# Kernel tuning notes

Measured on AMD Instinct MI355X. Metric: run time of the kernel, lower is better.

## Reference

```python
import jax, jax.numpy as jnp
import numpy as np

B, T, C = 16, 2048, 1024
HEAD = 64

def setup_inputs() -> dict:
    key = jax.random.key(0)
    kx, kq, kk, kv = jax.random.split(key, 4)
    x = jax.random.normal(kx, (B, T, C), dtype=jnp.float32)
    s = 1.0 / np.sqrt(C)
    Wq = jax.random.normal(kq, (C, HEAD), dtype=jnp.float32) * s
    Wk = jax.random.normal(kk, (C, HEAD), dtype=jnp.float32) * s
    Wv = jax.random.normal(kv, (C, HEAD), dtype=jnp.float32) * s
    return {"x": x, "Wq": Wq, "Wk": Wk, "Wv": Wv}

def reference(x, Wq, Wk, Wv):
    Bb, Tt, Cc = x.shape
    q = jnp.einsum('btc,ch->bth', x, Wq)  # [B,T,H]
    k = jnp.einsum('btc,ch->bth', x, Wk)
    v = jnp.einsum('btc,ch->bth', x, Wv)
    # NOTE: source scales by C**-0.5 (n_embd), not head_size**-0.5
    scores = jnp.einsum('bth,bsh->bts', q, k) * (Cc ** -0.5)  # [B,T,T]
    causal = jnp.tril(jnp.ones((Tt, Tt), dtype=bool))
    scores = jnp.where(causal, scores, -jnp.inf)
    attn = jax.nn.softmax(scores, axis=-1)  # dropout p=0 -> identity
    out = jnp.einsum('bts,bsh->bth', attn, v)  # [B,T,H]
    return out
```

## Files before the change

### kernel.cpp

```cpp
#include <hip/hip_runtime.h>

typedef __bf16 bf16;
typedef __bf16 bf16x4 __attribute__((ext_vector_type(4)));
typedef __bf16 bf16x8 __attribute__((ext_vector_type(8)));
typedef float f32x4 __attribute__((ext_vector_type(4)));

#define TT_ 2048
#define CC_ 1024
#define HH_ 64

#define SCALE2 0.045084221f

__global__ __launch_bounds__(256) void prep_w(const float* __restrict__ Wq,
                                              const float* __restrict__ Wk,
                                              const float* __restrict__ Wv,
                                              bf16* __restrict__ Wt) {
    __shared__ bf16 Ls[64 * 65];
    const int m  = blockIdx.x >> 4;
    const int k0 = (blockIdx.x & 15) * 64;
    const float* W = (m == 0) ? Wq : (m == 1) ? Wk : Wv;
    const int tid = threadIdx.x;
    #pragma unroll
    for (int j = 0; j < 4; ++j) {
        int idx = tid + 256 * j;
        int r   = idx >> 4;
        int c4  = (idx & 15) * 4;
        float4 w = *(const float4*)&W[(size_t)(k0 + r) * HH_ + c4];
        Ls[r * 65 + c4 + 0] = (bf16)w.x;
        Ls[r * 65 + c4 + 1] = (bf16)w.y;
        Ls[r * 65 + c4 + 2] = (bf16)w.z;
        Ls[r * 65 + c4 + 3] = (bf16)w.w;
    }
    __syncthreads();
    #pragma unroll
    for (int j = 0; j < 4; ++j) {
        int idx = tid + 256 * j;
        int n   = idx >> 4;
        int kc  = (idx & 15) * 4;
        bf16x4 v;
        #pragma unroll
        for (int i = 0; i < 4; ++i) v[i] = Ls[(kc + i) * 65 + n];
        *(bf16x4*)&Wt[m * 65536 + n * 1024 + k0 + kc] = v;
    }
}

__global__ __launch_bounds__(256) void qkv_kernel(const float* __restrict__ x,
                                                  const bf16* __restrict__ Wt,
                                                  bf16* __restrict__ qb,
                                                  bf16* __restrict__ kb,
                                                  bf16* __restrict__ vt) {
    __shared__ __align__(16) bf16 Xs[2][64 * 72];
    const int tid  = threadIdx.x;
    const int wave = tid >> 6;
    const int lane = tid & 15;
    const int quad = (tid & 63) >> 4;
    const int m0   = blockIdx.x * 64;

    f32x4 acc[4][3];
    #pragma unroll
    for (int i = 0; i < 4; ++i)
        #pragma unroll
        for (int j = 0; j < 3; ++j) acc[i][j] = f32x4{0.f, 0.f, 0.f, 0.f};

    const int srow = tid >> 4;
    const int scol = (tid & 15) * 4;

    float4 xr[4];
    #pragma unroll
    for (int rr = 0; rr < 4; ++rr)
        xr[rr] = *(const float4*)&x[(size_t)(m0 + srow + rr * 16) * CC_ + scol];
    #pragma unroll
    for (int rr = 0; rr < 4; ++rr) {
        bf16x4 bv = {(bf16)xr[rr].x, (bf16)xr[rr].y, (bf16)xr[rr].z, (bf16)xr[rr].w};
        *(bf16x4*)&Xs[0][(srow + rr * 16) * 72 + scol] = bv;
    }

    for (int kbi = 0; kbi < 16; ++kbi) {
        const int cur = kbi & 1;
        const int k0  = kbi * 64;
        __syncthreads();
        if (kbi < 15) {
            #pragma unroll
            for (int rr = 0; rr < 4; ++rr)
                xr[rr] = *(const float4*)&x[(size_t)(m0 + srow + rr * 16) * CC_ + k0 + 64 + scol];
        }
        bf16x8 bfr[2][3];
        #pragma unroll
        for (int step = 0; step < 2; ++step)
            #pragma unroll
            for (int ct = 0; ct < 3; ++ct)
                bfr[step][ct] = *(const bf16x8*)&Wt[(size_t)(wave * 48 + ct * 16 + lane) * 1024 + k0 + step * 32 + quad * 8];
        bf16x8 afr[2][4];
        #pragma unroll
        for (int step = 0; step < 2; ++step)
            #pragma unroll
            for (int rt = 0; rt < 4; ++rt)
                afr[step][rt] = *(const bf16x8*)&Xs[cur][(rt * 16 + lane) * 72 + step * 32 + quad * 8];
        #pragma unroll
        for (int step = 0; step < 2; ++step)
            #pragma unroll
            for (int ct = 0; ct < 3; ++ct)
                #pragma unroll
                for (int rt = 0; rt < 4; ++rt)
                    acc[rt][ct] = __builtin_amdgcn_mfma_f32_16x16x32_bf16(afr[step][rt], bfr[step][ct], acc[rt][ct], 0, 0, 0);
        if (kbi < 15) {
            #pragma unroll
            for (int rr = 0; rr < 4; ++rr) {
                bf16x4 bv = {(bf16)xr[rr].x, (bf16)xr[rr].y, (bf16)xr[rr].z, (bf16)xr[rr].w};
                *(bf16x4*)&Xs[cur ^ 1][(srow + rr * 16) * 72 + scol] = bv;
            }
        }
    }

    const int bb = m0 >> 11;
    const int t0 = m0 & 2047;
    __syncthreads();
    #pragma unroll
    for (int ct = 0; ct < 3; ++ct) {
        int c0 = wave * 48 + ct * 16;
        if (c0 < 128) {
            bf16* outp = (c0 < 64) ? qb : kb;
            int h = (c0 & 63) + lane;
            #pragma unroll
            for (int rt = 0; rt < 4; ++rt)
                #pragma unroll
                for (int r = 0; r < 4; ++r)
                    outp[(size_t)(m0 + rt * 16 + quad * 4 + r) * HH_ + h] = (bf16)acc[rt][ct][r];
        } else {
            int h = (c0 - 128) + lane;
            #pragma unroll
            for (int rt = 0; rt < 4; ++rt)
                #pragma unroll
                for (int r = 0; r < 4; ++r)
                    Xs[0][(rt * 16 + quad * 4 + r) * 72 + h] = (bf16)acc[rt][ct][r];
        }
    }
    __syncthreads();
    {
        int h  = tid >> 2;
        int tc = (tid & 3) * 16;
        bf16x8 v0, v1;
        #pragma unroll
        for (int i = 0; i < 8; ++i) v0[i] = Xs[0][(tc + i) * 72 + h];
        #pragma unroll
        for (int i = 0; i < 8; ++i) v1[i] = Xs[0][(tc + 8 + i) * 72 + h];
        bf16* dst = &vt[(size_t)bb * HH_ * TT_ + (size_t)h * TT_ + t0 + tc];
        *(bf16x8*)dst = v0;
        *(bf16x8*)(dst + 8) = v1;
    }
}

__global__ __launch_bounds__(256) void attn_kernel(const bf16* __restrict__ qb,
                                                   const bf16* __restrict__ kb,
                                                   const bf16* __restrict__ vt,
                                                   bf16* __restrict__ PO,
                                                   float* __restrict__ PL) {
    __shared__ __align__(16) bf16 Ks[128 * 72];
    __shared__ __align__(16) bf16 Vs[64 * 136];
    __shared__ __align__(16) bf16 Ps[4][16 * 136];

    const int tid  = threadIdx.x;
    const int wave = tid >> 6;
    const int lane = tid & 15;
    const int quad = (tid & 63) >> 4;
    const int idx = blockIdx.x;
    const int bb  = blockIdx.y;
    int seg, qi;
    if (idx < 32)      { seg = 0; qi = idx; }
    else if (idx < 56) { seg = 1; qi = idx - 24; }
    else if (idx < 72) { seg = 2; qi = idx - 40; }
    else               { seg = 3; qi = idx - 48; }
    const int q0   = qi * 64;
    const int qrow = q0 + wave * 16;
    const int nch   = (seg < (qi >> 3)) ? 4 : (((qi & 7) + 2) >> 1);
    const int diagc = (seg == (qi >> 3)) ? nch - 1 : -1;

    bf16x8 aq[2];
    #pragma unroll
    for (int step = 0; step < 2; ++step)
        aq[step] = *(const bf16x8*)&qb[(size_t)(bb * TT_ + qrow + lane) * HH_ + step * 32 + quad * 8];

    f32x4 o_acc[4];
    #pragma unroll
    for (int ht = 0; ht < 4; ++ht) o_acc[ht] = f32x4{0.f, 0.f, 0.f, 0.f};
    float l_lane[4] = {0.f, 0.f, 0.f, 0.f};

    for (int c = 0; c < nch; ++c) {
        const int s0 = seg * 512 + c * 128;
        __syncthreads();
        #pragma unroll
        for (int j = 0; j < 4; ++j) {
            int ch = tid + 256 * j;
            int row = ch >> 3, c8 = (ch & 7) * 8;
            *(bf16x8*)&Ks[row * 72 + c8] =
                *(const bf16x8*)&kb[(size_t)(bb * TT_ + s0 + row) * HH_ + c8];
        }
        #pragma unroll
        for (int j = 0; j < 4; ++j) {
            int ch = tid + 256 * j;
            int h = ch >> 4, c8 = (ch & 15) * 8;
            *(bf16x8*)&Vs[h * 136 + c8] =
                *(const bf16x8*)&vt[(size_t)bb * HH_ * TT_ + (size_t)h * TT_ + s0 + c8];
        }
        __syncthreads();

        f32x4 sfr[8];
        #pragma unroll
        for (int nt = 0; nt < 8; ++nt) sfr[nt] = f32x4{0.f, 0.f, 0.f, 0.f};
        #pragma unroll
        for (int step = 0; step < 2; ++step)
            #pragma unroll
            for (int nt = 0; nt < 8; ++nt) {
                bf16x8 bk = *(const bf16x8*)&Ks[(nt * 16 + lane) * 72 + step * 32 + quad * 8];
                sfr[nt] = __builtin_amdgcn_mfma_f32_16x16x32_bf16(aq[step], bk, sfr[nt], 0, 0, 0);
            }

        const bool msk = (c == diagc);
        #pragma unroll
        for (int r = 0; r < 4; ++r) {
            const int rowg = qrow + quad * 4 + r;
            #pragma unroll
            for (int nt = 0; nt < 8; ++nt) {
                float e = __builtin_amdgcn_exp2f(sfr[nt][r] * SCALE2);
                if (msk && (s0 + nt * 16 + lane) > rowg) e = 0.f;
                sfr[nt][r] = e;
                l_lane[r] += e;
            }
        }

        #pragma unroll
        for (int nt = 0; nt < 8; ++nt)
            #pragma unroll
            for (int r = 0; r < 4; ++r)
                Ps[wave][(quad * 4 + r) * 136 + nt * 16 + lane] = (bf16)sfr[nt][r];

        #pragma unroll
        for (int step = 0; step < 4; ++step) {
            bf16x8 ap = *(const bf16x8*)&Ps[wave][lane * 136 + step * 32 + quad * 8];
            #pragma unroll
            for (int ht = 0; ht < 4; ++ht) {
                bf16x8 bv = *(const bf16x8*)&Vs[(ht * 16 + lane) * 136 + step * 32 + quad * 8];
                o_acc[ht] = __builtin_amdgcn_mfma_f32_16x16x32_bf16(ap, bv, o_acc[ht], 0, 0, 0);
            }
        }
    }

    const size_t p = (size_t)bb * 80 + idx;
    #pragma unroll
    for (int ht = 0; ht < 4; ++ht)
        #pragma unroll
        for (int r = 0; r < 4; ++r)
            PO[p * 4096 + (size_t)(wave * 16 + quad * 4 + r) * 64 + ht * 16 + lane] = (bf16)o_acc[ht][r];
    #pragma unroll
    for (int r = 0; r < 4; ++r) {
        float l = l_lane[r];
        l += __shfl_xor(l, 1);
        l += __shfl_xor(l, 2);
        l += __shfl_xor(l, 4);
        l += __shfl_xor(l, 8);
        if (lane == 0) PL[p * 64 + wave * 16 + quad * 4 + r] = l;
    }
}

__global__ __launch_bounds__(256) void combine_kernel(const bf16* __restrict__ PO,
                                                      const float* __restrict__ PL,
                                                      float* __restrict__ out) {
    const int qi = blockIdx.x, bb = blockIdx.y;
    const int tid = threadIdx.x;
    const int r  = tid >> 2;
    const int cb = (tid & 3) * 16;
    const int ns = (qi >> 3) + 1;
    const int off[4] = {0, 32, 56, 72};

    float acc[16];
    #pragma unroll
    for (int i = 0; i < 16; ++i) acc[i] = 0.f;
    float l = 0.f;
    for (int s = 0; s < ns; ++s) {
        const size_t p = (size_t)bb * 80 + off[s] + qi - 8 * s;
        l += PL[p * 64 + r];
        const bf16* po = &PO[p * 4096 + (size_t)r * 64 + cb];
        bf16x8 a0 = *(const bf16x8*)po;
        bf16x8 a1 = *(const bf16x8*)(po + 8);
        #pragma unroll
        for (int i = 0; i < 8; ++i) { acc[i] += (float)a0[i]; acc[8 + i] += (float)a1[i]; }
    }
    const float inv = 1.0f / l;
    float* dst = &out[(size_t)(bb * TT_ + qi * 64 + r) * HH_ + cb];
    #pragma unroll
    for (int v = 0; v < 4; ++v) {
        float4 o = {acc[v * 4] * inv, acc[v * 4 + 1] * inv, acc[v * 4 + 2] * inv, acc[v * 4 + 3] * inv};
        *(float4*)(dst + v * 4) = o;
    }
}

extern "C" void kernel_launch(void* const* d_in, const int* in_sizes, int n_in,
                              void* d_out, int out_size, void* d_ws, size_t ws_size,
                              hipStream_t stream) {
    const float* x  = (const float*)d_in[0];
    const float* Wq = (const float*)d_in[1];
    const float* Wk = (const float*)d_in[2];
    const float* Wv = (const float*)d_in[3];
    float* out = (float*)d_out;

    char* ws = (char*)d_ws;
    bf16*  qb = (bf16*)(ws);
    bf16*  kb = (bf16*)(ws + 4194304);
    bf16*  vt = (bf16*)(ws + 8388608);
    bf16*  Wt = (bf16*)(ws + 12582912);
    bf16*  PO = (bf16*)(ws + 12976128);
    float* PL = (float*)(ws + 23461888);

    prep_w<<<48, 256, 0, stream>>>(Wq, Wk, Wv, Wt);
    qkv_kernel<<<512, 256, 0, stream>>>(x, Wt, qb, kb, vt);
    attn_kernel<<<dim3(80, 16), 256, 0, stream>>>(qb, kb, vt, PO, PL);
    combine_kernel<<<dim3(32, 16), 256, 0, stream>>>(PO, PL, out);
}
```

Baseline: 258.6 us.

## Load x directly into registers in QKV, halve rows per block, alias P with K in LDS

The QKV projection now uses 32 rows per block across twice as many blocks. Each wave loads and converts its x fragments straight from global memory instead of staging them through double-buffered shared memory, and a min-blocks launch bound is added. In attention, the per-wave P buffer now reuses the K tile's shared memory, with an extra barrier, to cut LDS footprint and raise occupancy. The cost is redundant global reads of x across the four waves (relying on cache) and an additional synchronisation per chunk.

```diff
diff --git a/kernel.cpp b/kernel.cpp
--- a/kernel.cpp
+++ b/kernel.cpp
@@ -44,77 +44,56 @@
     }
 }
 
-__global__ __launch_bounds__(256) void qkv_kernel(const float* __restrict__ x,
-                                                  const bf16* __restrict__ Wt,
-                                                  bf16* __restrict__ qb,
-                                                  bf16* __restrict__ kb,
-                                                  bf16* __restrict__ vt) {
-    __shared__ __align__(16) bf16 Xs[2][64 * 72];
+__global__ __launch_bounds__(256, 4) void qkv_kernel(const float* __restrict__ x,
+                                                     const bf16* __restrict__ Wt,
+                                                     bf16* __restrict__ qb,
+                                                     bf16* __restrict__ kb,
+                                                     bf16* __restrict__ vt) {
+    __shared__ __align__(16) bf16 Vsm[32 * 72];
     const int tid  = threadIdx.x;
     const int wave = tid >> 6;
     const int lane = tid & 15;
     const int quad = (tid & 63) >> 4;
-    const int m0   = blockIdx.x * 64;
-
-    f32x4 acc[4][3];
-    #pragma unroll
-    for (int i = 0; i < 4; ++i)
+    const int m0   = blockIdx.x * 32;
+
+    f32x4 acc[2][3];
+    #pragma unroll
+    for (int i = 0; i < 2; ++i)
         #pragma unroll
         for (int j = 0; j < 3; ++j) acc[i][j] = f32x4{0.f, 0.f, 0.f, 0.f};
 
-    const int srow = tid >> 4;
-    const int scol = (tid & 15) * 4;
-
-    float4 xr[4];
-    #pragma unroll
-    for (int rr = 0; rr < 4; ++rr)
-        xr[rr] = *(const float4*)&x[(size_t)(m0 + srow + rr * 16) * CC_ + scol];
-    #pragma unroll
-    for (int rr = 0; rr < 4; ++rr) {
-        bf16x4 bv = {(bf16)xr[rr].x, (bf16)xr[rr].y, (bf16)xr[rr].z, (bf16)xr[rr].w};
-        *(bf16x4*)&Xs[0][(srow + rr * 16) * 72 + scol] = bv;
-    }
-
+    #pragma unroll 4
     for (int kbi = 0; kbi < 16; ++kbi) {
-        const int cur = kbi & 1;
-        const int k0  = kbi * 64;
-        __syncthreads();
-        if (kbi < 15) {
-            #pragma unroll
-            for (int rr = 0; rr < 4; ++rr)
-                xr[rr] = *(const float4*)&x[(size_t)(m0 + srow + rr * 16) * CC_ + k0 + 64 + scol];
-        }
+        const int k0 = kbi * 64;
+        bf16x8 afr[2][2];
+        #pragma unroll
+        for (int rt = 0; rt < 2; ++rt)
+            #pragma unroll
+            for (int step = 0; step < 2; ++step) {
+                const float* xp = &x[(size_t)(m0 + rt * 16 + lane) * CC_ + k0 + step * 32 + quad * 8];
+                float4 a0 = *(const float4*)xp;
+                float4 a1 = *(const float4*)(xp + 4);
+                bf16x8 af = {(bf16)a0.x, (bf16)a0.y, (bf16)a0.z, (bf16)a0.w,
+                             (bf16)a1.x, (bf16)a1.y, (bf16)a1.z, (bf16)a1.w};
+                afr[rt][step] = af;
+            }
         bf16x8 bfr[2][3];
         #pragma unroll
         for (int step = 0; step < 2; ++step)
             #pragma unroll
             for (int ct = 0; ct < 3; ++ct)
                 bfr[step][ct] = *(const bf16x8*)&Wt[(size_t)(wave * 48 + ct * 16 + lane) * 1024 + k0 + step * 32 + quad * 8];
-        bf16x8 afr[2][4];
-        #pragma unroll
-        for (int step = 0; step < 2; ++step)
-            #pragma unroll
-            for (int rt = 0; rt < 4; ++rt)
-                afr[step][rt] = *(const bf16x8*)&Xs[cur][(rt * 16 + lane) * 72 + step * 32 + quad * 8];
         #pragma unroll
         for (int step = 0; step < 2; ++step)
             #pragma unroll
             for (int ct = 0; ct < 3; ++ct)
                 #pragma unroll
-                for (int rt = 0; rt < 4; ++rt)
-                    acc[rt][ct] = __builtin_amdgcn_mfma_f32_16x16x32_bf16(afr[step][rt], bfr[step][ct], acc[rt][ct], 0, 0, 0);
-        if (kbi < 15) {
-            #pragma unroll
-            for (int rr = 0; rr < 4; ++rr) {
-                bf16x4 bv = {(bf16)xr[rr].x, (bf16)xr[rr].y, (bf16)xr[rr].z, (bf16)xr[rr].w};
-                *(bf16x4*)&Xs[cur ^ 1][(srow + rr * 16) * 72 + scol] = bv;
-            }
-        }
+                for (int rt = 0; rt < 2; ++rt)
+                    acc[rt][ct] = __builtin_amdgcn_mfma_f32_16x16x32_bf16(afr[rt][step], bfr[step][ct], acc[rt][ct], 0, 0, 0);
     }
 
     const int bb = m0 >> 11;
     const int t0 = m0 & 2047;
-    __syncthreads();
     #pragma unroll
     for (int ct = 0; ct < 3; ++ct) {
         int c0 = wave * 48 + ct * 16;
@@ -122,31 +101,27 @@
             bf16* outp = (c0 < 64) ? qb : kb;
             int h = (c0 & 63) + lane;
             #pragma unroll
-            for (int rt = 0; rt < 4; ++rt)
+            for (int rt = 0; rt < 2; ++rt)
                 #pragma unroll
                 for (int r = 0; r < 4; ++r)
                     outp[(size_t)(m0 + rt * 16 + quad * 4 + r) * HH_ + h] = (bf16)acc[rt][ct][r];
         } else {
             int h = (c0 - 128) + lane;
             #pragma unroll
-            for (int rt = 0; rt < 4; ++rt)
+            for (int rt = 0; rt < 2; ++rt)
                 #pragma unroll
                 for (int r = 0; r < 4; ++r)
-                    Xs[0][(rt * 16 + quad * 4 + r) * 72 + h] = (bf16)acc[rt][ct][r];
+                    Vsm[(rt * 16 + quad * 4 + r) * 72 + h] = (bf16)acc[rt][ct][r];
         }
     }
     __syncthreads();
     {
         int h  = tid >> 2;
-        int tc = (tid & 3) * 16;
-        bf16x8 v0, v1;
-        #pragma unroll
-        for (int i = 0; i < 8; ++i) v0[i] = Xs[0][(tc + i) * 72 + h];
-        #pragma unroll
-        for (int i = 0; i < 8; ++i) v1[i] = Xs[0][(tc + 8 + i) * 72 + h];
-        bf16* dst = &vt[(size_t)bb * HH_ * TT_ + (size_t)h * TT_ + t0 + tc];
-        *(bf16x8*)dst = v0;
-        *(bf16x8*)(dst + 8) = v1;
+        int tc = (tid & 3) * 8;
+        bf16x8 v;
+        #pragma unroll
+        for (int i = 0; i < 8; ++i) v[i] = Vsm[(tc + i) * 72 + h];
+        *(bf16x8*)&vt[(size_t)bb * HH_ * TT_ + (size_t)h * TT_ + t0 + tc] = v;
     }
 }
 
@@ -155,9 +130,8 @@
                                                    const bf16* __restrict__ vt,
                                                    bf16* __restrict__ PO,
                                                    float* __restrict__ PL) {
-    __shared__ __align__(16) bf16 Ks[128 * 72];
+    __shared__ __align__(16) bf16 KsPs[128 * 72];
     __shared__ __align__(16) bf16 Vs[64 * 136];
-    __shared__ __align__(16) bf16 Ps[4][16 * 136];
 
     const int tid  = threadIdx.x;
     const int wave = tid >> 6;
@@ -174,6 +148,7 @@
     const int qrow = q0 + wave * 16;
     const int nch   = (seg < (qi >> 3)) ? 4 : (((qi & 7) + 2) >> 1);
     const int diagc = (seg == (qi >> 3)) ? nch - 1 : -1;
+    bf16* Pw = KsPs + wave * (16 * 136);
 
     bf16x8 aq[2];
     #pragma unroll
@@ -192,7 +167,7 @@
         for (int j = 0; j < 4; ++j) {
             int ch = tid + 256 * j;
             int row = ch >> 3, c8 = (ch & 7) * 8;
-            *(bf16x8*)&Ks[row * 72 + c8] =
+            *(bf16x8*)&KsPs[row * 72 + c8] =
                 *(const bf16x8*)&kb[(size_t)(bb * TT_ + s0 + row) * HH_ + c8];
         }
         #pragma unroll
@@ -211,7 +186,7 @@
         for (int step = 0; step < 2; ++step)
             #pragma unroll
             for (int nt = 0; nt < 8; ++nt) {
-                bf16x8 bk = *(const bf16x8*)&Ks[(nt * 16 + lane) * 72 + step * 32 + quad * 8];
+                bf16x8 bk = *(const bf16x8*)&KsPs[(nt * 16 + lane) * 72 + step * 32 + quad * 8];
                 sfr[nt] = __builtin_amdgcn_mfma_f32_16x16x32_bf16(aq[step], bk, sfr[nt], 0, 0, 0);
             }
 
@@ -228,15 +203,16 @@
             }
         }
 
+        __syncthreads();
         #pragma unroll
         for (int nt = 0; nt < 8; ++nt)
             #pragma unroll
             for (int r = 0; r < 4; ++r)
-                Ps[wave][(quad * 4 + r) * 136 + nt * 16 + lane] = (bf16)sfr[nt][r];
+                Pw[(quad * 4 + r) * 136 + nt * 16 + lane] = (bf16)sfr[nt][r];
 
         #pragma unroll
         for (int step = 0; step < 4; ++step) {
-            bf16x8 ap = *(const bf16x8*)&Ps[wave][lane * 136 + step * 32 + quad * 8];
+            bf16x8 ap = *(const bf16x8*)&Pw[lane * 136 + step * 32 + quad * 8];
             #pragma unroll
             for (int ht = 0; ht < 4; ++ht) {
                 bf16x8 bv = *(const bf16x8*)&Vs[(ht * 16 + lane) * 136 + step * 32 + quad * 8];
@@ -312,7 +288,7 @@
     float* PL = (float*)(ws + 23461888);
 
     prep_w<<<48, 256, 0, stream>>>(Wq, Wk, Wv, Wt);
-    qkv_kernel<<<512, 256, 0, stream>>>(x, Wt, qb, kb, vt);
+    qkv_kernel<<<1024, 256, 0, stream>>>(x, Wt, qb, kb, vt);
     attn_kernel<<<dim3(80, 16), 256, 0, stream>>>(qb, kb, vt, PO, PL);
     combine_kernel<<<dim3(32, 16), 256, 0, stream>>>(PO, PL, out);
 }
```

Result: slower. 312.2 us (+20.7%).
